# Performance work log

Measured on AMD Instinct MI355X. Metric: run time of the kernel, lower is better.

## Reference

```python
import jax, jax.numpy as jnp
import numpy as np

H = 128            # hardcoded image side in the torch module
TOL = 1e-3         # forward() default tol
MAX_DEPTH = 8      # init kwarg (reduced from 200 for bounded runtime)
LRELU = 0.1        # LeakyReLU negative slope


def _conv(x, w, b, pad):
    # x: [B,Cin,H,H], w: [Cout,Cin,kh,kw]
    y = jax.lax.conv_general_dilated(
        x, w, (1, 1), [(pad, pad), (pad, pad)],
        dimension_numbers=('NCHW', 'OIHW', 'NCHW'))
    if b is not None:
        y = y + b[None, :, None, None]
    return y


def _leaky(x):
    return jnp.where(x >= 0, x, LRELU * x)


def _build_apply_T(d, A, w1, b1, w2, b2, w3, b3, wK, delta, alpha, lambd, beta):
    B = d.shape[0]
    Kc = wK.shape[0]
    dcol = d.reshape(B, -1).T                      # [m, B]
    # ConvTranspose2d(K->1, k=3, pad=1) with weight := convK.weight is the
    # adjoint of convK: regular conv with spatially flipped, channel-swapped kernel.
    wKt = jnp.transpose(jnp.flip(wK, (2, 3)), (1, 0, 2, 3))  # [1,K,3,3]

    def K_op(xk):                                  # [N,B] -> [K*N,B]
        x4 = xk.T.reshape(B, 1, H, H)
        return _conv(x4, wK, None, 1).reshape(B, -1).T

    def Kt_op(pk):                                 # [K*N,B] -> [N,B]
        p4 = pk.T.reshape(B, Kc, H, H)
        return _conv(p4, wKt, None, 1).reshape(B, -1).T

    def R_op(pk):                                  # learned residual denoiser
        p = pk.T.reshape(B, Kc, H, H)
        p = p + _leaky(_conv(p, w1, b1, 2))
        p = p + _leaky(_conv(p, w2, b2, 2))
        p = p + _leaky(_conv(p, w3, b3, 2))
        return p.reshape(B, -1).T

    def ball_proj(w):                              # eval-mode projection
        de = jnp.exp(delta)                        # (1,) -> broadcasts over batch
        dist = jnp.maximum(jnp.linalg.norm(w - dcol, axis=0), 1e-10)
        dn = jnp.linalg.norm(dcol, axis=0)
        scale = jnp.minimum(jnp.ones_like(dist), de * dn / dist)
        return dcol + scale * (w - dcol)

    a = jnp.clip(alpha, 0.0, 2.0)
    bta = jnp.clip(beta, 0.0, 2.0)
    lam = jnp.clip(lambd, 0.0, 2.0)

    def apply_T(x):                                # x: [B,1,H,H]
        xk = x.reshape(B, -1).T                    # [N,B]
        Kxk = K_op(xk)
        # torch: pk = K(xk); pk += lambd*(nuk1 + alpha*(K(xk)-pk)) with nuk1=0
        # and pk==K(xk), so the update is identity -> pk = Kxk.
        pk = R_op(Kxk)
        Axk = A @ xk                               # [m,B]
        # torch: wk = A@xk; temp = wk + lambd*(nuk2 + alpha*(Axk-wk)) = Axk.
        wk = ball_proj(Axk)
        nuk1p = a * (Kxk - pk)
        nuk2p = a * (Axk - wk)
        # nuk1 = nuk2 = 0, so 2*nuk_plus - nuk = 2*nuk_plus
        rk = Kt_op(2.0 * nuk1p) + A.T @ (2.0 * nuk2p)
        xk_new = jnp.clip(xk - bta * rk, 0.0, 1.0)
        return xk_new.T.reshape(B, 1, H, H)

    return apply_T


def setup_inputs() -> dict:
    key = jax.random.key(0)
    ks = jax.random.split(key, 10)
    B, M, N_side, Kc = 8, 4096, 128, 2
    d = jax.random.normal(ks[0], (B, M), jnp.float32)
    A = jax.random.normal(ks[1], (M, N_side * N_side), jnp.float32) / 128.0
    w1 = jax.random.normal(ks[2], (Kc, Kc, 5, 5), jnp.float32) * 0.05
    w2 = jax.random.normal(ks[3], (Kc, Kc, 5, 5), jnp.float32) * 0.05
    w3 = jax.random.normal(ks[4], (Kc, Kc, 5, 5), jnp.float32) * 0.05
    b1 = jnp.zeros((Kc,), jnp.float32)
    b2 = jnp.zeros((Kc,), jnp.float32)
    b3 = jnp.zeros((Kc,), jnp.float32)
    wK = jax.random.normal(ks[5], (Kc, 1, 3, 3), jnp.float32) * 0.1
    return {
        'd': d, 'A': A,
        'w1': w1, 'b1': b1, 'w2': w2, 'b2': b2, 'w3': w3, 'b3': b3,
        'wK': wK,
        'delta': jnp.full((1,), -5.0, jnp.float32),
        'alpha': jnp.full((1,), 0.1, jnp.float32),
        'lambd': jnp.full((1,), 0.1, jnp.float32),
        'beta': jnp.full((1,), 0.1, jnp.float32),
    }


def reference(d, A, w1, b1, w2, b2, w3, b3, wK, delta, alpha, lambd, beta):
    B = d.shape[0]
    apply_T = _build_apply_T(d, A, w1, b1, w2, b2, w3, b3, wK,
                             delta, alpha, lambd, beta)
    x0 = jnp.zeros((B, 1, H, H), d.dtype)
    xp0 = jnp.full((B, 1, H, H), jnp.inf, d.dtype)

    def cond(state):
        x, xp, k = state
        res = jnp.max(jnp.linalg.norm((x - xp).reshape(B, -1), axis=1))
        return (res > TOL) & (k < MAX_DEPTH)

    def body(state):
        x, xp, k = state
        return (apply_T(x), x, k + 1)

    x_star, _, _ = jax.lax.while_loop(cond, body, (x0, xp0, jnp.int32(0)))
    # final differentiable application T(x*)
    return apply_T(x_star)
```

## Files before the change

### kernel.cpp

```cpp
#include <hip/hip_runtime.h>
#include <math.h>

#define HH 128
#define NPIX 16384
#define BB 8
#define MM 4096
#define NN 16384
#define KC 2
#define LRELU_S 0.1f

typedef __attribute__((ext_vector_type(8))) short bf16x8;
typedef __attribute__((ext_vector_type(4))) float f32x4;

__device__ __forceinline__ float leaky_(float v){ return v >= 0.f ? v : LRELU_S*v; }
__device__ __forceinline__ float clamp01(float v){ return fminf(fmaxf(v, 0.f), 1.f); }
__device__ __forceinline__ float clamp02(float v){ return fminf(fmaxf(v, 0.f), 2.f); }
__device__ __forceinline__ unsigned short f2bf(float f){
  unsigned u = __float_as_uint(f);
  u = (u + 0x7FFFu + ((u >> 16) & 1u)) >> 16;
  return (unsigned short)u;
}

__global__ __launch_bounds__(256) void k_prep(const float* __restrict__ A_,
                                              unsigned short* __restrict__ Abf,
                                              unsigned short* __restrict__ Atp){
  __shared__ float lds[64][65];
  int bm = blockIdx.x >> 8, bn = blockIdx.x & 255;
  int m0 = bm*64, n0 = bn*64;
  int t = threadIdx.x;
  for (int i=t; i<64*16; i+=256){
    int r = i >> 4, c4 = i & 15;
    float4 v = *(const float4*)&A_[(size_t)(m0+r)*NN + n0 + c4*4];
    lds[r][c4*4+0]=v.x; lds[r][c4*4+1]=v.y; lds[r][c4*4+2]=v.z; lds[r][c4*4+3]=v.w;
  }
  __syncthreads();
  for (int i=t; i<64*16; i+=256){
    int r = i >> 4, c4 = i & 15;
    unsigned short o[4];
    for (int j=0;j<4;++j) o[j] = f2bf(lds[r][c4*4+j]);
    *(uint2*)&Abf[(size_t)(m0+r)*NN + n0 + c4*4] = *(uint2*)o;
  }
  for (int i=t; i<8*64; i+=256){
    int mbl = i >> 6, nl = i & 63;
    unsigned short o[8];
    for (int j=0;j<8;++j) o[j] = f2bf(lds[mbl*8+j][nl]);
    *(uint4*)&Atp[((size_t)(m0/8 + mbl)*NN + n0 + nl)*8] = *(uint4*)o;
  }
}

__global__ __launch_bounds__(256) void k_dn(const float* __restrict__ d, float* __restrict__ dn){
  int b = blockIdx.x, t = threadIdx.x;
  float ss = 0.f;
  for (int m=t; m<MM; m+=256){ float v = d[b*MM + m]; ss += v*v; }
  #pragma unroll
  for (int off=32; off; off>>=1) ss += __shfl_down(ss, off);
  __shared__ float red[4];
  if ((t & 63) == 0) red[t>>6] = ss;
  __syncthreads();
  if (t == 0) dn[b] = sqrtf(red[0]+red[1]+red[2]+red[3]);
}

__global__ __launch_bounds__(256) void k_conv_chain(const float* __restrict__ x,
    const float* __restrict__ wK, const float* __restrict__ w1, const float* __restrict__ b1,
    const float* __restrict__ w2, const float* __restrict__ b2,
    const float* __restrict__ w3, const float* __restrict__ b3,
    const float* __restrict__ alpha, float* __restrict__ rk){
  __shared__ float xs[24][128];
  __shared__ float bufA[2][22][128];
  __shared__ float bufB[2][18][128];
  __shared__ float wKs[18], w1s[100], w2s[100], w3s[100], bs[3][2];
  __shared__ float twoa;
  int blk = blockIdx.x;
  int b = blk >> 4, slab = blk & 15, r0 = slab*8;
  int t = threadIdx.x;
  for (int i=t;i<18;i+=256) wKs[i]=wK[i];
  for (int i=t;i<100;i+=256){ w1s[i]=w1[i]; w2s[i]=w2[i]; w3s[i]=w3[i]; }
  if (t<2){ bs[0][t]=b1[t]; bs[1][t]=b2[t]; bs[2][t]=b3[t]; }
  if (t==0) twoa = 2.f*clamp02(alpha[0]);
  for (int idx=t; idx<24*128; idx+=256){
    int i = idx>>7, j = idx&127, ir = r0-8+i;
    xs[i][j] = ((unsigned)ir < 128u) ? x[b*NPIX + ir*HH + j] : 0.f;
  }
  __syncthreads();
  for (int c=0;c<2;++c)
    for (int idx=t; idx<22*128; idx+=256){
      int i = idx>>7, j = idx&127, ir = r0-7+i;
      float s = 0.f;
      if ((unsigned)ir < 128u){
        #pragma unroll
        for (int di=0;di<3;++di){
          #pragma unroll
          for (int dj=0;dj<3;++dj){
            int jj = j+dj-1;
            if ((unsigned)jj < 128u) s += xs[i+di][jj]*wKs[(c*3+di)*3+dj];
          }
        }
      }
      bufA[c][i][j] = s;
    }
  __syncthreads();
  for (int o=0;o<2;++o)
    for (int idx=t; idx<18*128; idx+=256){
      int i = idx>>7, j = idx&127, ir = r0-5+i;
      float v = 0.f;
      if ((unsigned)ir < 128u){
        float s = bs[0][o];
        #pragma unroll
        for (int c=0;c<2;++c)
          #pragma unroll
          for (int di=0;di<5;++di)
            #pragma unroll
            for (int dj=0;dj<5;++dj){
              int jj = j+dj-2;
              if ((unsigned)jj < 128u) s += bufA[c][i+di][jj]*w1s[(o*2+c)*25+di*5+dj];
            }
        v = bufA[o][i+2][j] + leaky_(s);
      }
      bufB[o][i][j] = v;
    }
  __syncthreads();
  for (int o=0;o<2;++o)
    for (int idx=t; idx<14*128; idx+=256){
      int i = idx>>7, j = idx&127, ir = r0-3+i;
      float v = 0.f;
      if ((unsigned)ir < 128u){
        float s = bs[1][o];
        #pragma unroll
        for (int c=0;c<2;++c)
          #pragma unroll
          for (int di=0;di<5;++di)
            #pragma unroll
            for (int dj=0;dj<5;++dj){
              int jj = j+dj-2;
              if ((unsigned)jj < 128u) s += bufB[c][i+di][jj]*w2s[(o*2+c)*25+di*5+dj];
            }
        v = bufB[o][i+2][j] + leaky_(s);
      }
      bufA[o][i][j] = v;
    }
  __syncthreads();
  for (int o=0;o<2;++o)
    for (int idx=t; idx<10*128; idx+=256){
      int i = idx>>7, j = idx&127, ir = r0-1+i;
      float v = 0.f;
      if ((unsigned)ir < 128u){
        float s = bs[2][o];
        #pragma unroll
        for (int c=0;c<2;++c)
          #pragma unroll
          for (int di=0;di<5;++di)
            #pragma unroll
            for (int dj=0;dj<5;++dj){
              int jj = j+dj-2;
              if ((unsigned)jj < 128u) s += bufA[c][i+di][jj]*w3s[(o*2+c)*25+di*5+dj];
            }
        v = bufA[o][i+2][j] + leaky_(s);
      }
      bufB[o][i][j] = v;
    }
  __syncthreads();
  for (int c=0;c<2;++c)
    for (int idx=t; idx<10*128; idx+=256){
      int i = idx>>7, j = idx&127, ir = r0-1+i;
      float v = 0.f;
      if ((unsigned)ir < 128u){
        float kx = 0.f;
        #pragma unroll
        for (int di=0;di<3;++di)
          #pragma unroll
          for (int dj=0;dj<3;++dj){
            int jj = j+dj-1;
            if ((unsigned)jj < 128u) kx += xs[i+6+di][jj]*wKs[(c*3+di)*3+dj];
          }
        v = twoa*(kx - bufB[c][i][j]);
      }
      bufA[c][i][j] = v;
    }
  __syncthreads();
  for (int idx=t; idx<8*128; idx+=256){
    int i = idx>>7, j = idx&127, ir = r0+i;
    float s = 0.f;
    #pragma unroll
    for (int c=0;c<2;++c)
      #pragma unroll
      for (int di=0;di<3;++di)
        #pragma unroll
        for (int dj=0;dj<3;++dj){
          int jj = j+dj-1;
          if ((unsigned)jj < 128u) s += bufA[c][i+di][jj]*wKs[(c*3+(2-di))*3+(2-dj)];
        }
    rk[b*NPIX + ir*HH + j] = s;
  }
}

__global__ __launch_bounds__(512) void k_gemm1mf(const unsigned short* __restrict__ Abf,
    const unsigned short* __restrict__ xtt, const float* __restrict__ d_,
    float* __restrict__ e_, float* __restrict__ d2p){
  int mt = blockIdx.x;
  int w = threadIdx.x >> 6;
  int lane = threadIdx.x & 63;
  int kg = lane >> 4, col = lane & 15;
  const unsigned short* Ap = Abf + (size_t)(mt*16 + col)*NN + w*2048 + kg*8;
  const unsigned short* Bp = xtt + ((size_t)(w*256 + kg)*16 + col)*8;
  f32x4 acc = {0.f,0.f,0.f,0.f};
  #pragma unroll 8
  for (int s=0; s<64; ++s){
    bf16x8 a = *(const bf16x8*)(Ap + s*32);
    bf16x8 b = *(const bf16x8*)(Bp + s*512);
    acc = __builtin_amdgcn_mfma_f32_16x16x32_bf16(a, b, acc, 0, 0, 0);
  }
  __shared__ float part[8][16][16];
  __shared__ float p2[16][16];
  #pragma unroll
  for (int j=0;j<4;++j) part[w][kg*4+j][col] = acc[j];
  __syncthreads();
  int t = threadIdx.x;
  if (t < 256){
    int r = t >> 4, b = t & 15;
    float s = 0.f;
    #pragma unroll
    for (int w2=0; w2<8; ++w2) s += part[w2][r][b];
    int m = mt*16 + r;
    float ee = s - ((b < 8) ? d_[b*MM + m] : 0.f);
    e_[m*16 + b] = ee;
    p2[r][b] = (b < 8) ? ee*ee : 0.f;
  }
  __syncthreads();
  if (t < 8){
    float s2 = 0.f;
    #pragma unroll
    for (int r2=0;r2<16;++r2) s2 += p2[r2][t];
    d2p[mt*8 + t] = s2;
  }
}

__global__ __launch_bounds__(256) void k_zt(const float* __restrict__ e_,
    const float* __restrict__ d2p, const float* __restrict__ dn,
    const float* __restrict__ delta, const float* __restrict__ alpha,
    unsigned short* __restrict__ zt){
  __shared__ float red[32][8];
  __shared__ float cf[8];
  int t = threadIdx.x;
  {
    int b = t & 7, chunk = t >> 3;
    float s = 0.f;
    #pragma unroll
    for (int i=0;i<8;++i) s += d2p[(chunk + 32*i)*8 + b];
    red[chunk][b] = s;
  }
  __syncthreads();
  if (t < 8){
    float s2 = 0.f;
    #pragma unroll
    for (int c=0;c<32;++c) s2 += red[c][t];
    float dist = fmaxf(sqrtf(s2), 1e-10f);
    float de = expf(delta[0]);
    float a = clamp02(alpha[0]);
    float scale = fminf(1.f, de*dn[t]/dist);
    cf[t] = 2.f*a*(1.f - scale);
  }
  __syncthreads();
  int m0 = blockIdx.x*128;
  for (int idx=t; idx<128*16; idx+=256){
    int ml = idx >> 4, b = idx & 15, m = m0 + ml;
    float v = (b < 8) ? cf[b]*e_[m*16 + b] : 0.f;
    zt[(size_t)(m>>3)*128 + b*8 + (m&7)] = f2bf(v);
  }
}

__global__ __launch_bounds__(64) void k_gemm2mf(const unsigned short* __restrict__ Atp,
    const unsigned short* __restrict__ zt, float* __restrict__ up){
  int blk = blockIdx.x;
  int nt = blk >> 1, ms = blk & 1;
  int lane = threadIdx.x;
  int kg = lane >> 4, nc = lane & 15;
  const unsigned short* Ap = zt  + ((size_t)(ms*256 + kg)*16 + nc)*8;
  const unsigned short* Bp = Atp + ((size_t)(ms*256 + kg)*NN + nt*16 + nc)*8;
  f32x4 acc = {0.f,0.f,0.f,0.f};
  #pragma unroll 8
  for (int s=0; s<64; ++s){
    bf16x8 a = *(const bf16x8*)(Ap + (size_t)s*512);
    bf16x8 b = *(const bf16x8*)(Bp + (size_t)s*4*NN*8);
    acc = __builtin_amdgcn_mfma_f32_16x16x32_bf16(a, b, acc, 0, 0, 0);
  }
  #pragma unroll
  for (int j=0;j<4;++j)
    up[(size_t)(ms*16 + kg*4 + j)*NN + nt*16 + nc] = acc[j];
}

__global__ __launch_bounds__(256) void k_combine2(const float* __restrict__ up,
    const float* __restrict__ rk, const float* __restrict__ beta,
    float* __restrict__ x, unsigned short* __restrict__ xtt){
  int gid = blockIdx.x*256 + threadIdx.x;
  int b = gid >> 11, nb = gid & 2047, n0 = nb*8;
  if (b >= 8){
    uint4 z = {0,0,0,0};
    *(uint4*)&xtt[(size_t)(nb*16 + b)*8] = z;
    return;
  }
  float bta = clamp02(beta[0]);
  float xv[8]; unsigned short o[8];
  #pragma unroll
  for (int j=0;j<8;++j){
    float v = rk[b*NPIX + n0 + j]
            + up[(size_t)(0*16 + b)*NN + n0 + j]
            + up[(size_t)(1*16 + b)*NN + n0 + j];
    xv[j] = clamp01(x[b*NPIX + n0 + j] - bta*v);
    o[j] = f2bf(xv[j]);
  }
  #pragma unroll
  for (int j=0;j<8;++j) x[b*NPIX + n0 + j] = xv[j];
  *(uint4*)&xtt[(size_t)(nb*16 + b)*8] = *(uint4*)o;
}

extern "C" void kernel_launch(void* const* d_in, const int* in_sizes, int n_in,
                              void* d_out, int out_size, void* d_ws, size_t ws_size,
                              hipStream_t stream) {
  const float* d_d   = (const float*)d_in[0];
  const float* d_A   = (const float*)d_in[1];
  const float* w1    = (const float*)d_in[2];
  const float* b1    = (const float*)d_in[3];
  const float* w2    = (const float*)d_in[4];
  const float* b2    = (const float*)d_in[5];
  const float* w3    = (const float*)d_in[6];
  const float* b3    = (const float*)d_in[7];
  const float* wK    = (const float*)d_in[8];
  const float* delta = (const float*)d_in[9];
  const float* alpha = (const float*)d_in[10];
  const float* beta  = (const float*)d_in[12];

  char* p = (char*)d_ws;
  unsigned short* Abf = (unsigned short*)p; p += (size_t)MM*NN*2;
  unsigned short* Atp = (unsigned short*)p; p += (size_t)MM*NN*2;
  unsigned short* xtt = (unsigned short*)p; p += (size_t)2048*16*8*2;
  unsigned short* zt  = (unsigned short*)p; p += (size_t)512*16*8*2;
  float* x   = (float*)p; p += (size_t)BB*NPIX*4;
  float* rk1 = (float*)p; p += (size_t)BB*NPIX*4;
  float* e_  = (float*)p; p += (size_t)MM*16*4;
  float* up  = (float*)p; p += (size_t)2*16*NN*4;
  float* d2p = (float*)p; p += (size_t)256*8*4;
  float* dnb = (float*)p; p += 64;

  k_prep<<<64*256, 256, 0, stream>>>(d_A, Abf, Atp);
  k_dn<<<BB, 256, 0, stream>>>(d_d, dnb);
  hipMemsetAsync(x, 0, (size_t)BB*NPIX*4, stream);
  hipMemsetAsync(xtt, 0, (size_t)2048*16*8*2, stream);

  for (int it=0; it<9; ++it){
    k_conv_chain<<<128, 256, 0, stream>>>(x, wK, w1, b1, w2, b2, w3, b3, alpha, rk1);
    k_gemm1mf<<<256, 512, 0, stream>>>(Abf, xtt, d_d, e_, d2p);
    k_zt<<<32, 256, 0, stream>>>(e_, d2p, dnb, delta, alpha, zt);
    k_gemm2mf<<<2048, 64, 0, stream>>>(Atp, zt, up);
    k_combine2<<<128, 256, 0, stream>>>(up, rk1, beta, x, xtt);
  }

  hipMemcpyAsync(d_out, x, (size_t)BB*NPIX*4, hipMemcpyDeviceToDevice, stream);
}
```

Baseline: 1.467 ms.

## Drop transposed A copy; compute A^T z with vector FMA over row-major bf16 A

Removes the packed transposed bf16 copy of A, so the prep kernel becomes a plain elementwise fp32-to-bf16 conversion and writes half as much data. The separate z-scaling kernel and the MFMA transpose-GEMM are replaced by one kernel. It computes the ball-projection coefficients, stages scaled residuals in LDS, and accumulates A^T z with scalar FMAs, streaming coalesced rows of A. Partial sums over 32 M-slices are written to a larger buffer and reduced in the combine kernel. This trades tensor-core use and fewer partial sums for less setup traffic and one fewer launch per iteration.

```diff
diff --git a/kernel.cpp b/kernel.cpp
--- a/kernel.cpp
+++ b/kernel.cpp
@@ -6,7 +6,6 @@
 #define BB 8
 #define MM 4096
 #define NN 16384
-#define KC 2
 #define LRELU_S 0.1f
 
 typedef __attribute__((ext_vector_type(8))) short bf16x8;
@@ -20,32 +19,18 @@
   u = (u + 0x7FFFu + ((u >> 16) & 1u)) >> 16;
   return (unsigned short)u;
 }
+__device__ __forceinline__ float bf2f(unsigned short s){
+  return __uint_as_float(((unsigned)s) << 16);
+}
 
 __global__ __launch_bounds__(256) void k_prep(const float* __restrict__ A_,
-                                              unsigned short* __restrict__ Abf,
-                                              unsigned short* __restrict__ Atp){
-  __shared__ float lds[64][65];
-  int bm = blockIdx.x >> 8, bn = blockIdx.x & 255;
-  int m0 = bm*64, n0 = bn*64;
-  int t = threadIdx.x;
-  for (int i=t; i<64*16; i+=256){
-    int r = i >> 4, c4 = i & 15;
-    float4 v = *(const float4*)&A_[(size_t)(m0+r)*NN + n0 + c4*4];
-    lds[r][c4*4+0]=v.x; lds[r][c4*4+1]=v.y; lds[r][c4*4+2]=v.z; lds[r][c4*4+3]=v.w;
-  }
-  __syncthreads();
-  for (int i=t; i<64*16; i+=256){
-    int r = i >> 4, c4 = i & 15;
-    unsigned short o[4];
-    for (int j=0;j<4;++j) o[j] = f2bf(lds[r][c4*4+j]);
-    *(uint2*)&Abf[(size_t)(m0+r)*NN + n0 + c4*4] = *(uint2*)o;
-  }
-  for (int i=t; i<8*64; i+=256){
-    int mbl = i >> 6, nl = i & 63;
-    unsigned short o[8];
-    for (int j=0;j<8;++j) o[j] = f2bf(lds[mbl*8+j][nl]);
-    *(uint4*)&Atp[((size_t)(m0/8 + mbl)*NN + n0 + nl)*8] = *(uint4*)o;
-  }
+                                              unsigned short* __restrict__ Abf){
+  size_t i = ((size_t)blockIdx.x*256 + threadIdx.x)*8;
+  float4 v0 = *(const float4*)&A_[i];
+  float4 v1 = *(const float4*)&A_[i+4];
+  unsigned short o[8] = { f2bf(v0.x), f2bf(v0.y), f2bf(v0.z), f2bf(v0.w),
+                          f2bf(v1.x), f2bf(v1.y), f2bf(v1.z), f2bf(v1.w) };
+  *(uint4*)&Abf[i] = *(uint4*)o;
 }
 
 __global__ __launch_bounds__(256) void k_dn(const float* __restrict__ d, float* __restrict__ dn){
@@ -88,13 +73,12 @@
       float s = 0.f;
       if ((unsigned)ir < 128u){
         #pragma unroll
-        for (int di=0;di<3;++di){
+        for (int di=0;di<3;++di)
           #pragma unroll
           for (int dj=0;dj<3;++dj){
             int jj = j+dj-1;
             if ((unsigned)jj < 128u) s += xs[i+di][jj]*wKs[(c*3+di)*3+dj];
           }
-        }
       }
       bufA[c][i][j] = s;
     }
@@ -234,58 +218,63 @@
   }
 }
 
-__global__ __launch_bounds__(256) void k_zt(const float* __restrict__ e_,
-    const float* __restrict__ d2p, const float* __restrict__ dn,
-    const float* __restrict__ delta, const float* __restrict__ alpha,
-    unsigned short* __restrict__ zt){
-  __shared__ float red[32][8];
+#define G2_MS 32
+#define G2_MC 128
+#define G2_NB 16
+#define G2_NC 1024
+__global__ __launch_bounds__(256) void k_gemm2v(const unsigned short* __restrict__ Abf,
+    const float* __restrict__ e_, const float* __restrict__ d2p,
+    const float* __restrict__ dn, const float* __restrict__ delta,
+    const float* __restrict__ alpha, float* __restrict__ up){
+  __shared__ float zs[BB][G2_MC];
+  __shared__ float red[8][8];
   __shared__ float cf[8];
+  int blk = blockIdx.x;
+  int ms = blk >> 4, nb = blk & 15;
+  int m0 = ms*G2_MC, n0 = nb*G2_NC;
   int t = threadIdx.x;
-  {
-    int b = t & 7, chunk = t >> 3;
+  if (t < 64){
+    int b = t & 7, part = t >> 3;
     float s = 0.f;
-    #pragma unroll
-    for (int i=0;i<8;++i) s += d2p[(chunk + 32*i)*8 + b];
-    red[chunk][b] = s;
+    for (int i=0;i<32;++i) s += d2p[(part*32+i)*8 + b];
+    red[part][b] = s;
   }
   __syncthreads();
   if (t < 8){
     float s2 = 0.f;
     #pragma unroll
-    for (int c=0;c<32;++c) s2 += red[c][t];
+    for (int p=0;p<8;++p) s2 += red[p][t];
     float dist = fmaxf(sqrtf(s2), 1e-10f);
     float de = expf(delta[0]);
     float a = clamp02(alpha[0]);
-    float scale = fminf(1.f, de*dn[t]/dist);
-    cf[t] = 2.f*a*(1.f - scale);
-  }
-  __syncthreads();
-  int m0 = blockIdx.x*128;
-  for (int idx=t; idx<128*16; idx+=256){
-    int ml = idx >> 4, b = idx & 15, m = m0 + ml;
-    float v = (b < 8) ? cf[b]*e_[m*16 + b] : 0.f;
-    zt[(size_t)(m>>3)*128 + b*8 + (m&7)] = f2bf(v);
-  }
-}
-
-__global__ __launch_bounds__(64) void k_gemm2mf(const unsigned short* __restrict__ Atp,
-    const unsigned short* __restrict__ zt, float* __restrict__ up){
-  int blk = blockIdx.x;
-  int nt = blk >> 1, ms = blk & 1;
-  int lane = threadIdx.x;
-  int kg = lane >> 4, nc = lane & 15;
-  const unsigned short* Ap = zt  + ((size_t)(ms*256 + kg)*16 + nc)*8;
-  const unsigned short* Bp = Atp + ((size_t)(ms*256 + kg)*NN + nt*16 + nc)*8;
-  f32x4 acc = {0.f,0.f,0.f,0.f};
-  #pragma unroll 8
-  for (int s=0; s<64; ++s){
-    bf16x8 a = *(const bf16x8*)(Ap + (size_t)s*512);
-    bf16x8 b = *(const bf16x8*)(Bp + (size_t)s*4*NN*8);
-    acc = __builtin_amdgcn_mfma_f32_16x16x32_bf16(a, b, acc, 0, 0, 0);
-  }
-  #pragma unroll
-  for (int j=0;j<4;++j)
-    up[(size_t)(ms*16 + kg*4 + j)*NN + nt*16 + nc] = acc[j];
+    cf[t] = 2.f*a*(1.f - fminf(1.f, de*dn[t]/dist));
+  }
+  __syncthreads();
+  for (int i=t; i<BB*G2_MC; i+=256){
+    int ml = i >> 3, b = i & 7;
+    zs[b][ml] = cf[b]*e_[(m0+ml)*16 + b];
+  }
+  __syncthreads();
+  float4 acc[BB];
+  #pragma unroll
+  for (int b=0;b<BB;++b){ acc[b].x=0.f; acc[b].y=0.f; acc[b].z=0.f; acc[b].w=0.f; }
+  const unsigned short* Ap = Abf + (size_t)m0*NN + n0 + t*4;
+  #pragma unroll 4
+  for (int ml=0; ml<G2_MC; ++ml){
+    uint2 araw = *(const uint2*)(Ap + (size_t)ml*NN);
+    float a0 = bf2f((unsigned short)(araw.x & 0xffff));
+    float a1 = bf2f((unsigned short)(araw.x >> 16));
+    float a2 = bf2f((unsigned short)(araw.y & 0xffff));
+    float a3 = bf2f((unsigned short)(araw.y >> 16));
+    #pragma unroll
+    for (int b=0;b<BB;++b){
+      float s = zs[b][ml];
+      acc[b].x += a0*s; acc[b].y += a1*s; acc[b].z += a2*s; acc[b].w += a3*s;
+    }
+  }
+  #pragma unroll
+  for (int b=0;b<BB;++b)
+    *(float4*)&up[((size_t)ms*BB + b)*NN + n0 + t*4] = acc[b];
 }
 
 __global__ __launch_bounds__(256) void k_combine2(const float* __restrict__ up,
@@ -299,13 +288,25 @@
     return;
   }
   float bta = clamp02(beta[0]);
+  float acc[8];
+  {
+    float4 r0 = *(const float4*)&rk[b*NPIX + n0];
+    float4 r1 = *(const float4*)&rk[b*NPIX + n0 + 4];
+    acc[0]=r0.x; acc[1]=r0.y; acc[2]=r0.z; acc[3]=r0.w;
+    acc[4]=r1.x; acc[5]=r1.y; acc[6]=r1.z; acc[7]=r1.w;
+  }
+  #pragma unroll 8
+  for (int ms=0; ms<G2_MS; ++ms){
+    const float* u = &up[((size_t)ms*BB + b)*NN + n0];
+    float4 u0 = *(const float4*)u;
+    float4 u1 = *(const float4*)(u+4);
+    acc[0]+=u0.x; acc[1]+=u0.y; acc[2]+=u0.z; acc[3]+=u0.w;
+    acc[4]+=u1.x; acc[5]+=u1.y; acc[6]+=u1.z; acc[7]+=u1.w;
+  }
   float xv[8]; unsigned short o[8];
   #pragma unroll
   for (int j=0;j<8;++j){
-    float v = rk[b*NPIX + n0 + j]
-            + up[(size_t)(0*16 + b)*NN + n0 + j]
-            + up[(size_t)(1*16 + b)*NN + n0 + j];
-    xv[j] = clamp01(x[b*NPIX + n0 + j] - bta*v);
+    xv[j] = clamp01(x[b*NPIX + n0 + j] - bta*acc[j]);
     o[j] = f2bf(xv[j]);
   }
   #pragma unroll
@@ -331,17 +332,15 @@
 
   char* p = (char*)d_ws;
   unsigned short* Abf = (unsigned short*)p; p += (size_t)MM*NN*2;
-  unsigned short* Atp = (unsigned short*)p; p += (size_t)MM*NN*2;
   unsigned short* xtt = (unsigned short*)p; p += (size_t)2048*16*8*2;
-  unsigned short* zt  = (unsigned short*)p; p += (size_t)512*16*8*2;
   float* x   = (float*)p; p += (size_t)BB*NPIX*4;
   float* rk1 = (float*)p; p += (size_t)BB*NPIX*4;
   float* e_  = (float*)p; p += (size_t)MM*16*4;
-  float* up  = (float*)p; p += (size_t)2*16*NN*4;
+  float* up  = (float*)p; p += (size_t)G2_MS*BB*NN*4;
   float* d2p = (float*)p; p += (size_t)256*8*4;
   float* dnb = (float*)p; p += 64;
 
-  k_prep<<<64*256, 256, 0, stream>>>(d_A, Abf, Atp);
+  k_prep<<<MM*NN/(256*8), 256, 0, stream>>>(d_A, Abf);
   k_dn<<<BB, 256, 0, stream>>>(d_d, dnb);
   hipMemsetAsync(x, 0, (size_t)BB*NPIX*4, stream);
   hipMemsetAsync(xtt, 0, (size_t)2048*16*8*2, stream);
@@ -349,8 +348,7 @@
   for (int it=0; it<9; ++it){
     k_conv_chain<<<128, 256, 0, stream>>>(x, wK, w1, b1, w2, b2, w3, b3, alpha, rk1);
     k_gemm1mf<<<256, 512, 0, stream>>>(Abf, xtt, d_d, e_, d2p);
-    k_zt<<<32, 256, 0, stream>>>(e_, d2p, dnb, delta, alpha, zt);
-    k_gemm2mf<<<2048, 64, 0, stream>>>(Atp, zt, up);
+    k_gemm2v<<<G2_MS*G2_NB, 256, 0, stream>>>(Abf, e_, d2p, dnb, delta, alpha, up);
     k_combine2<<<128, 256, 0, stream>>>(up, rk1, beta, x, xtt);
   }
 
```

Measured after the change: 1.498 ms. +2.2%, slower.
